# Kernel tuning notes

Hardware: AMD Instinct MI355X
Metric: run time of the kernel (lower is better)

## Reference

```python
import jax, jax.numpy as jnp
import numpy as np

BATCH, SEQ, VOCAB, EMB, UNITS = 128, 80, 10000, 100, 2048

def setup_inputs() -> dict:
    key = jax.random.key(0)
    ks = jax.random.split(key, 12)
    s = 0.02
    return {
        "tokens": jax.random.randint(ks[0], (BATCH, SEQ), 0, VOCAB, dtype=jnp.int32),
        "emb": jax.random.normal(ks[1], (VOCAB, EMB), jnp.float32) * s,
        "W0": jax.random.normal(ks[2], (EMB, 4 * UNITS), jnp.float32) * s,
        "U0": jax.random.normal(ks[3], (UNITS, 4 * UNITS), jnp.float32) * s,
        "b0": jnp.zeros((4 * UNITS,), jnp.float32),
        "W1": jax.random.normal(ks[4], (UNITS, 4 * UNITS), jnp.float32) * s,
        "U1": jax.random.normal(ks[5], (UNITS, 4 * UNITS), jnp.float32) * s,
        "b1": jnp.zeros((4 * UNITS,), jnp.float32),
        "Wd": jax.random.normal(ks[6], (UNITS, UNITS), jnp.float32) * s,
        "bd": jnp.zeros((UNITS,), jnp.float32),
        "Wo": jax.random.normal(ks[7], (UNITS, 1), jnp.float32) * s,
        "bo": jnp.zeros((1,), jnp.float32),
    }

def _lstm_step(x, h, c, W, U, b):
    # Keras LSTMCell gate order: i, f, g(candidate), o
    z = x @ W + h @ U + b  # [B, 4U]
    i, f, g, o = jnp.split(z, 4, axis=-1)
    c_new = jax.nn.sigmoid(f) * c + jax.nn.sigmoid(i) * jnp.tanh(g)
    h_new = jax.nn.sigmoid(o) * jnp.tanh(c_new)
    return h_new, c_new

def reference(tokens, emb, W0, U0, b0, W1, U1, b1, Wd, bd, Wo, bo):
    x = emb[tokens]                      # [B, T, E]
    xs = jnp.swapaxes(x, 0, 1)           # [T, B, E] for scan over time
    B = tokens.shape[0]
    U = U0.shape[0]
    init = (jnp.zeros((B, U), x.dtype), jnp.zeros((B, U), x.dtype),
            jnp.zeros((B, U), x.dtype), jnp.zeros((B, U), x.dtype))

    def step(carry, xt):
        h0, c0, h1, c1 = carry
        h0, c0 = _lstm_step(xt, h0, c0, W0, U0, b0)
        h1, c1 = _lstm_step(h0, h1, c1, W1, U1, b1)
        return (h0, c0, h1, c1), None

    (h0, c0, h1, c1), _ = jax.lax.scan(step, init, xs)
    # out layer: Dense(units) -> Dropout(inference: identity) -> ReLU -> Dense(1)
    y = jax.nn.relu(h1 @ Wd + bd)
    logit = y @ Wo + bo                  # [B, 1]
    return jax.nn.sigmoid(logit)
```

## Files before the change

### kernel.cpp

```cpp
#include <hip/hip_runtime.h>
#include <hip/hip_bf16.h>
#include <hip/hip_fp8.h>
#include <cstdint>

#define B_   128
#define T_   80
#define E_   100
#define U_   2048
#define G4_  8192

#define SA_    16.0f
#define SB4_   64.0f
#define INV_S_ (1.0f / 1024.0f)
#define SCL1_  0x7F7F7F7F

typedef __attribute__((ext_vector_type(4))) float f32x4;
typedef __attribute__((ext_vector_type(8))) int   i32x8;
typedef __attribute__((ext_vector_type(4))) int   i32x4;

__device__ __forceinline__ unsigned char f2fp8(float x) {
    __hip_fp8_e4m3 q(x);
    return q.__x;
}

__device__ __forceinline__ unsigned int q4(float x) {
    float a = fabsf(x);
    unsigned int s = (x < 0.f) ? 8u : 0u;
    unsigned int c = a < 0.25f ? 0u : a < 0.75f ? 1u : a < 1.25f ? 2u :
                     a < 1.75f ? 3u : a < 2.5f  ? 4u : a < 3.5f  ? 5u :
                     a < 5.0f  ? 6u : 7u;
    return s | c;
}

__device__ __forceinline__ unsigned char pk4(float v0, float v1) {
#if __has_builtin(__builtin_amdgcn_cvt_scalef32_pk_fp4_f32)
    unsigned int w = __builtin_amdgcn_cvt_scalef32_pk_fp4_f32(0u, v0, v1, 1.0f, 0);
    return (unsigned char)(w & 0xFF);
#else
    return (unsigned char)(q4(v0) | (q4(v1) << 4));
#endif
}

__global__ __launch_bounds__(256)
void embed_pack(const int* __restrict__ tokens, const float* __restrict__ emb,
                unsigned char* __restrict__ Xp) {
    int gtid = blockIdx.x * 256 + threadIdx.x;
    if (gtid >= T_ * 8 * 64 * 4) return;
    int eb   = gtid & 3;
    int lane = (gtid >> 2) & 63;
    int mtg  = (gtid >> 8) & 7;
    int t    = gtid >> 11;
    int row  = (mtg >> 2) * 64 + (mtg & 3) * 16 + (lane & 15);
    const float* erow = emb + (size_t)tokens[row * T_ + t] * E_;
    unsigned char v[8];
#pragma unroll
    for (int j = 0; j < 8; ++j) {
        int k = (lane >> 4) * 32 + eb * 8 + j;
        v[j] = (k < E_) ? f2fp8(SA_ * erow[k]) : 0;
    }
    unsigned char* dst = Xp + ((size_t)(t * 8 + mtg)) * 2048 + lane * 32 + eb * 8;
    *reinterpret_cast<uint2*>(dst) = *reinterpret_cast<const uint2*>(v);
}

__global__ __launch_bounds__(256)
void pack_all(const float* __restrict__ W0, const float* __restrict__ U0,
              const float* __restrict__ W1, const float* __restrict__ U1,
              const float* __restrict__ Wd,
              unsigned char* __restrict__ W0p, unsigned char* __restrict__ U0p,
              unsigned char* __restrict__ W1p, unsigned char* __restrict__ U1p,
              unsigned char* __restrict__ Wdp) {
    __shared__ float4 st4[32][65];
    const float* stf = reinterpret_cast<const float*>(&st4[0][0]);
    const int tid = threadIdx.x;
    int blk = blockIdx.x;
    const float* W; int K, Ncols, NG, NW; unsigned char* out; int lb;
    if (blk < 2048)      { W = U0; K = U_; Ncols = G4_; NG = 4; NW = 16; out = U0p; lb = blk; }
    else if (blk < 4096) { W = W1; K = U_; Ncols = G4_; NG = 4; NW = 16; out = W1p; lb = blk - 2048; }
    else if (blk < 6144) { W = U1; K = U_; Ncols = G4_; NG = 4; NW = 16; out = U1p; lb = blk - 4096; }
    else if (blk < 6272) { W = W0; K = E_; Ncols = G4_; NG = 4; NW = 1;  out = W0p; lb = blk - 6144; }
    else                 { W = Wd; K = U_; Ncols = U_;  NG = 1; NW = 16; out = Wdp; lb = blk - 6272; }

    int Wm, kg, cg;
    if (NW == 1) { Wm = 0;        kg = lb & 3;         cg = lb >> 2; }
    else         { Wm = lb & 15;  kg = (lb >> 4) & 3;  cg = lb >> 6; }
    int g, utb;
    if (NG == 4) { g = cg >> 3; utb = (cg & 7) * 16; }
    else         { g = 0;       utb = cg * 16; }
    const int cb = cg * 256;

    {
        const int c4 = tid & 63;
        const int r0 = tid >> 6;
        float4 v[8];
#pragma unroll
        for (int p = 0; p < 8; ++p) {
            const int r = p * 4 + r0;
            const int k = Wm * 128 + kg * 32 + r;
            v[p] = make_float4(0.f, 0.f, 0.f, 0.f);
            if (k < K)
                v[p] = *reinterpret_cast<const float4*>(W + (size_t)k * Ncols + cb + c4 * 4);
        }
#pragma unroll
        for (int p = 0; p < 8; ++p) st4[p * 4 + r0][c4] = v[p];
    }
    __syncthreads();

    const int ut_l = tid >> 4;
    const int cl   = tid & 15;
    unsigned char v[16];
#pragma unroll
    for (int b = 0; b < 16; ++b) {
        float v0 = stf[((2 * b)     * 65 + (tid >> 2)) * 4 + (tid & 3)];
        float v1 = stf[((2 * b + 1) * 65 + (tid >> 2)) * 4 + (tid & 3)];
        v[b] = pk4(SB4_ * v0, SB4_ * v1);
    }
    const int ut = utb + ut_l;
    unsigned char* dst = out + (((size_t)(ut * NW + Wm)) * NG + g) * 1024 + (kg * 16 + cl) * 16;
    *reinterpret_cast<uint4*>(dst) = *reinterpret_cast<const uint4*>(v);
}

template<int NW0, int NW1>
__device__ __forceinline__ void ld_set(
    const unsigned char* __restrict__ a0, const unsigned char* __restrict__ a1,
    const unsigned char* __restrict__ b0, const unsigned char* __restrict__ b1,
    int w, i32x8 (&A)[4], i32x4 (&Bv)[4])
{
    if (w < NW0) {
#pragma unroll
        for (int mt = 0; mt < 4; ++mt)
            A[mt] = *reinterpret_cast<const i32x8*>(a0 + (size_t)(mt * NW0 + w) * 2048);
#pragma unroll
        for (int g = 0; g < 4; ++g)
            Bv[g] = *reinterpret_cast<const i32x4*>(b0 + (size_t)(w * 4 + g) * 1024);
    } else {
        int ww = w - NW0;
#pragma unroll
        for (int mt = 0; mt < 4; ++mt)
            A[mt] = *reinterpret_cast<const i32x8*>(a1 + (size_t)(mt * NW1 + ww) * 2048);
#pragma unroll
        for (int g = 0; g < 4; ++g)
            Bv[g] = *reinterpret_cast<const i32x4*>(b1 + (size_t)(ww * 4 + g) * 1024);
    }
}

__device__ __forceinline__ void ld_A(const unsigned char* __restrict__ a,
                                     int stride_nw, int w, i32x8 (&A)[4]) {
#pragma unroll
    for (int mt = 0; mt < 4; ++mt)
        A[mt] = *reinterpret_cast<const i32x8*>(a + (size_t)(mt * stride_nw + w) * 2048);
}

__device__ __forceinline__ void ld_B(const unsigned char* __restrict__ b,
                                     int w, i32x4 (&Bv)[4]) {
#pragma unroll
    for (int g = 0; g < 4; ++g)
        Bv[g] = *reinterpret_cast<const i32x4*>(b + (size_t)(w * 4 + g) * 1024);
}

__device__ __forceinline__ void mfma_set(f32x4 (&acc)[4][4], i32x8 (&A)[4], i32x4 (&Bv)[4]) {
    __builtin_amdgcn_s_setprio(1);
#pragma unroll
    for (int g = 0; g < 4; ++g) {
        i32x8 bf = {Bv[g][0], Bv[g][1], Bv[g][2], Bv[g][3], 0, 0, 0, 0};
#pragma unroll
        for (int mt = 0; mt < 4; ++mt)
            acc[g][mt] = __builtin_amdgcn_mfma_scale_f32_16x16x128_f8f6f4(
                A[mt], bf, acc[g][mt], 0, 4, 0, SCL1_, 0, SCL1_);
    }
    __builtin_amdgcn_s_setprio(0);
}

__device__ __forceinline__ void epilogue(
    f32x4 (&acc)[4][4], const float* __restrict__ bias,
    float* __restrict__ c, unsigned char* __restrict__ h_out,
    float (*zs)[4][64][17], int ut, int mh, int tid, int lane, int kq)
{
    const int lr = tid >> 3;
    const int u0 = (tid & 7) * 2;

    __syncthreads();
#pragma unroll
    for (int g = 0; g < 4; ++g)
#pragma unroll
        for (int mt = 0; mt < 4; ++mt)
#pragma unroll
            for (int r = 0; r < 4; ++r)
                zs[kq][g][mt * 16 + (lane >> 4) * 4 + r][lane & 15] = acc[g][mt][r];
    __syncthreads();

    float zg2[4][2];
#pragma unroll
    for (int g = 0; g < 4; ++g) {
        float s0 = 0.f, s1 = 0.f;
#pragma unroll
        for (int w8 = 0; w8 < 8; ++w8) {
            s0 += zs[w8][g][lr][u0];
            s1 += zs[w8][g][lr][u0 + 1];
        }
        zg2[g][0] = s0;
        zg2[g][1] = s1;
    }

    const int grow = mh * 64 + lr;
    const int unit = ut * 16 + u0;
    const float2 bi  = *reinterpret_cast<const float2*>(&bias[unit]);
    const float2 bfv = *reinterpret_cast<const float2*>(&bias[U_ + unit]);
    const float2 bgv = *reinterpret_cast<const float2*>(&bias[2 * U_ + unit]);
    const float2 bov = *reinterpret_cast<const float2*>(&bias[3 * U_ + unit]);
    float2 cv = *reinterpret_cast<float2*>(&c[(size_t)grow * U_ + unit]);

    float cn[2];
    unsigned char hv[2];
#pragma unroll
    for (int e = 0; e < 2; ++e) {
        float zi = zg2[0][e] * INV_S_ + (e ? bi.y : bi.x);
        float zf = zg2[1][e] * INV_S_ + (e ? bfv.y : bfv.x);
        float zg = zg2[2][e] * INV_S_ + (e ? bgv.y : bgv.x);
        float zo = zg2[3][e] * INV_S_ + (e ? bov.y : bov.x);
        float si = 1.f / (1.f + __expf(-zi));
        float sf = 1.f / (1.f + __expf(-zf));
        float so = 1.f / (1.f + __expf(-zo));
        float tg = tanhf(zg);
        float cc = sf * (e ? cv.y : cv.x) + si * tg;
        cn[e] = cc;
        hv[e] = f2fp8(SA_ * so * tanhf(cc));
    }
    *reinterpret_cast<float2*>(&c[(size_t)grow * U_ + unit]) = make_float2(cn[0], cn[1]);

    const int mt = lr >> 4;
    const int cl = lr & 15;
    const int Wh = unit >> 7;
    const int lg = (unit >> 5) & 3;
    const int e0 = unit & 31;
    size_t fr = (size_t)(mh * 4 + mt) * 16 + Wh;
    uchar2 hv2; hv2.x = hv[0]; hv2.y = hv[1];
    *reinterpret_cast<uchar2*>(&h_out[fr * 2048 + (lg * 16 + cl) * 32 + e0]) = hv2;
}

__global__ __launch_bounds__(512)
void lstm_l0_first(const unsigned char* __restrict__ Xp,
                   const unsigned char* __restrict__ W0p,
                   const unsigned char* __restrict__ U0p,
                   const float* __restrict__ b0,
                   float* __restrict__ c0,
                   const unsigned char* __restrict__ h0zero,
                   unsigned char* __restrict__ h0out) {
    __shared__ float zs[8][4][64][17];
    const int tid  = threadIdx.x;
    const int lane = tid & 63;
    const int kq   = tid >> 6;
    const int b    = blockIdx.x;
    const int s    = b >> 3;
    const int ut   = (b & 7) * 16 + (s >> 1);
    const int mh   = s & 1;

    const unsigned char* a0 = Xp     + ((size_t)(mh * 4) * 1)  * 2048 + lane * 32;
    const unsigned char* a1 = h0zero + ((size_t)(mh * 4) * 16) * 2048 + lane * 32;
    const unsigned char* p0 = W0p + ((size_t)(ut * 1)  * 4) * 1024 + lane * 16;
    const unsigned char* p1 = U0p + ((size_t)(ut * 16) * 4) * 1024 + lane * 16;

    f32x4 acc[4][4];
#pragma unroll
    for (int g = 0; g < 4; ++g)
#pragma unroll
        for (int mt = 0; mt < 4; ++mt) acc[g][mt] = f32x4{0.f, 0.f, 0.f, 0.f};

    i32x8 A0s[4], A1s[4], A2s[4];
    i32x4 B0s[4], B1s[4], B2s[4];
    ld_set<1, 16>(a0, a1, p0, p1, kq, A0s, B0s);
    ld_set<1, 16>(a0, a1, p0, p1, kq + 8, A1s, B1s);
    const bool tail = (kq + 16 < 17);
    if (tail) ld_set<1, 16>(a0, a1, p0, p1, kq + 16, A2s, B2s);
    mfma_set(acc, A0s, B0s);
    mfma_set(acc, A1s, B1s);
    if (tail) mfma_set(acc, A2s, B2s);

    epilogue(acc, b0, c0, h0out, zs, ut, mh, tid, lane, kq);
}

__global__ __launch_bounds__(512)
void lstm_phase(const unsigned char* __restrict__ Xp,
                const unsigned char* __restrict__ W0p,
                const unsigned char* __restrict__ U0p,
                const unsigned char* __restrict__ W1p,
                const unsigned char* __restrict__ U1p,
                const float* __restrict__ b0,
                const float* __restrict__ b1,
                float* __restrict__ c0, float* __restrict__ c1,
                const unsigned char* __restrict__ h0cur,
                unsigned char* __restrict__ h0next,
                const unsigned char* __restrict__ h1in,
                unsigned char* __restrict__ h1out,
                int k) {
    __shared__ float zs[8][4][64][17];
    const int tid  = threadIdx.x;
    const int lane = tid & 63;
    const int kq   = tid >> 6;
    const int b    = blockIdx.x;
    const int s    = b >> 3;
    const int ut   = (b & 7) * 16 + (s >> 1);
    const int mh   = s & 1;
    const bool hasL0 = (k + 1 < T_);

    const unsigned char* a0 = h0cur + ((size_t)(mh * 4) * 16) * 2048 + lane * 32;
    const unsigned char* a1 = h1in  + ((size_t)(mh * 4) * 16) * 2048 + lane * 32;
    const unsigned char* p0 = W1p + ((size_t)(ut * 16) * 4) * 1024 + lane * 16;
    const unsigned char* p1 = U1p + ((size_t)(ut * 16) * 4) * 1024 + lane * 16;
    const unsigned char* l0x  = Xp + (size_t)(k + 1) * 8 * 2048
                                   + ((size_t)(mh * 4) * 1) * 2048 + lane * 32;
    const unsigned char* l0b0 = W0p + ((size_t)(ut * 1)  * 4) * 1024 + lane * 16;
    const unsigned char* l0b1 = U0p + ((size_t)(ut * 16) * 4) * 1024 + lane * 16;

    f32x4 acc[4][4];
#pragma unroll
    for (int g = 0; g < 4; ++g)
#pragma unroll
        for (int mt = 0; mt < 4; ++mt) acc[g][mt] = f32x4{0.f, 0.f, 0.f, 0.f};

    i32x8 A0s[4], A1s[4], A2s[4], A3s[4];
    i32x4 B0s[4], B1s[4];
    ld_A(a0, 16, kq, A0s);       ld_B(p0, kq, B0s);
    ld_A(a0, 16, kq + 8, A1s);   ld_B(p0, kq + 8, B1s);
    ld_A(a1, 16, kq, A2s);
    mfma_set(acc, A0s, B0s);
    ld_B(p1, kq, B0s);
    ld_A(a1, 16, kq + 8, A3s);
    mfma_set(acc, A1s, B1s);
    ld_B(p1, kq + 8, B1s);
    mfma_set(acc, A2s, B0s);
    mfma_set(acc, A3s, B1s);

    i32x4 PB0[4], PB1[4], PBX[4];
    i32x8 PAX[4];
    if (hasL0) {
        ld_B(l0b1, kq, PB0);
        ld_B(l0b1, kq + 8, PB1);
        if (kq == 0) {
            ld_A(l0x, 1, 0, PAX);
            ld_B(l0b0, 0, PBX);
        }
    }

    epilogue(acc, b1, c1, h1out, zs, ut, mh, tid, lane, kq);

    if (hasL0) {
#pragma unroll
        for (int g = 0; g < 4; ++g)
#pragma unroll
            for (int mt = 0; mt < 4; ++mt) acc[g][mt] = f32x4{0.f, 0.f, 0.f, 0.f};

        mfma_set(acc, A0s, PB0);
        mfma_set(acc, A1s, PB1);
        if (kq == 0) mfma_set(acc, PAX, PBX);

        epilogue(acc, b0, c0, h0next, zs, ut, mh, tid, lane, kq);
    }
}

__global__ __launch_bounds__(256)
void head_mfma(const unsigned char* __restrict__ h1p,
               const unsigned char* __restrict__ Wdp,
               const float* __restrict__ bd, float* __restrict__ y) {
    const int lane = threadIdx.x & 63;
    const int w    = threadIdx.x >> 6;
    const int ut   = blockIdx.x & 127;
    const int mh   = blockIdx.x >> 7;

    const unsigned char* ap = h1p + ((size_t)(mh * 4) * 16) * 2048 + lane * 32;
    const unsigned char* wp = Wdp + ((size_t)(ut * 16)) * 1024 + lane * 16;

    f32x4 acc[4];
#pragma unroll
    for (int mt = 0; mt < 4; ++mt) acc[mt] = f32x4{0.f, 0.f, 0.f, 0.f};

#pragma unroll
    for (int wi = 0; wi < 4; ++wi) {
        const int W = w + wi * 4;
        i32x4 bq = *reinterpret_cast<const i32x4*>(wp + (size_t)W * 1024);
        i32x8 bf = {bq[0], bq[1], bq[2], bq[3], 0, 0, 0, 0};
#pragma unroll
        for (int mt = 0; mt < 4; ++mt) {
            i32x8 a = *reinterpret_cast<const i32x8*>(ap + (size_t)(mt * 16 + W) * 2048);
            acc[mt] = __builtin_amdgcn_mfma_scale_f32_16x16x128_f8f6f4(
                a, bf, acc[mt], 0, 4, 0, SCL1_, 0, SCL1_);
        }
    }

    __shared__ float zs[4][64][17];
#pragma unroll
    for (int mt = 0; mt < 4; ++mt)
#pragma unroll
        for (int r = 0; r < 4; ++r)
            zs[w][mt * 16 + (lane >> 4) * 4 + r][lane & 15] = acc[mt][r];
    __syncthreads();

    const int tid = threadIdx.x;
    const int lr  = tid >> 2;
    const int u4  = (tid & 3) * 4;
    const int grow = mh * 64 + lr;
    const int gu   = ut * 16 + u4;

    float4 r;
    float* rr = &r.x;
#pragma unroll
    for (int e = 0; e < 4; ++e) {
        float v = (zs[0][lr][u4 + e] + zs[1][lr][u4 + e] +
                   zs[2][lr][u4 + e] + zs[3][lr][u4 + e]) * INV_S_ + bd[gu + e];
        rr[e] = v > 0.f ? v : 0.f;
    }
    *reinterpret_cast<float4*>(&y[(size_t)grow * U_ + gu]) = r;
}

__global__ __launch_bounds__(256)
void head2(const float* __restrict__ y, const float* __restrict__ Wo,
           const float* __restrict__ bo, float* __restrict__ out) {
    __shared__ float red[256];
    const int b = blockIdx.x;
    const int tid = threadIdx.x;
    float s = 0.f;
    for (int u = tid; u < U_; u += 256) s += y[(size_t)b * U_ + u] * Wo[u];
    red[tid] = s;
    __syncthreads();
    for (int off = 128; off > 0; off >>= 1) {
        if (tid < off) red[tid] += red[tid + off];
        __syncthreads();
    }
    if (tid == 0) out[b] = 1.f / (1.f + __expf(-(red[0] + bo[0])));
}

extern "C" void kernel_launch(void* const* d_in, const int* in_sizes, int n_in,
                              void* d_out, int out_size, void* d_ws, size_t ws_size,
                              hipStream_t stream) {
    const int*   tokens = (const int*)  d_in[0];
    const float* emb    = (const float*)d_in[1];
    const float* W0     = (const float*)d_in[2];
    const float* U0     = (const float*)d_in[3];
    const float* b0     = (const float*)d_in[4];
    const float* W1     = (const float*)d_in[5];
    const float* U1     = (const float*)d_in[6];
    const float* b1     = (const float*)d_in[7];
    const float* Wd     = (const float*)d_in[8];
    const float* bd     = (const float*)d_in[9];
    const float* Wo     = (const float*)d_in[10];
    const float* bo     = (const float*)d_in[11];

    char* base = (char*)d_ws;
    unsigned char* h0a = (unsigned char*)(base + 0);
    unsigned char* h1a = (unsigned char*)(base + 262144);
    float*         c0  = (float*)        (base + 524288);
    float*         c1  = (float*)        (base + 1572864);
    unsigned char* h0b = (unsigned char*)(base + 2621440);
    unsigned char* h1b = (unsigned char*)(base + 2883584);
    unsigned char* Xp  = (unsigned char*)(base + 3145728);
    float*         yb  = (float*)        (base + 3145728);
    unsigned char* W0p = (unsigned char*)(base + 4456448);
    unsigned char* U0p = (unsigned char*)(base + 4980736);
    unsigned char* W1p = (unsigned char*)(base + 13369344);
    unsigned char* U1p = (unsigned char*)(base + 21757952);
    unsigned char* Wdp = (unsigned char*)(base + 30146560);

    hipMemsetAsync(d_ws, 0, 2621440, stream);

    embed_pack<<<(T_ * 8 * 64 * 4 + 255) / 256, 256, 0, stream>>>(tokens, emb, Xp);
    pack_all<<<6784, 256, 0, stream>>>(W0, U0, W1, U1, Wd,
                                       W0p, U0p, W1p, U1p, Wdp);

    lstm_l0_first<<<256, 512, 0, stream>>>(Xp, W0p, U0p, b0, c0, h0a, h0b);

    for (int k = 0; k < T_; ++k) {
        const unsigned char* h0cur  = (k & 1) ? h0a : h0b;
        unsigned char*       h0next = (k & 1) ? h0b : h0a;
        const unsigned char* h1in   = (k & 1) ? h1b : h1a;
        unsigned char*       h1out  = (k & 1) ? h1a : h1b;
        lstm_phase<<<256, 512, 0, stream>>>(Xp, W0p, U0p, W1p, U1p,
                                            b0, b1, c0, c1,
                                            h0cur, h0next, h1in, h1out, k);
    }
    head_mfma<<<256, 256, 0, stream>>>(h1a, Wdp, bd, yb);
    head2<<<B_, 256, 0, stream>>>(yb, Wo, bo, (float*)d_out);
}
```

Measured before the change: 1.044 ms.

## Quantize hidden states to FP4 and skip zero-state matmul in first step

Hidden states h0/h1 are now stored as packed FP4 (e2m1) with a larger scale instead of FP8, halving their bytes, and all recurrent and head MFMAs use the fp4×fp4 mode. The x-projection path stays FP8 and is rescaled by a constant to match the new accumulator scale. The first layer-0 step drops the U0·h multiply against the all-zero initial state. This cuts per-step load traffic and register footprint for A operands but coarsens hidden-state precision, which may hurt accuracy.

```diff
diff --git a/kernel.cpp b/kernel.cpp
--- a/kernel.cpp
+++ b/kernel.cpp
@@ -10,8 +10,10 @@
 #define G4_  8192
 
 #define SA_    16.0f
+#define SA4_   128.0f
 #define SB4_   64.0f
-#define INV_S_ (1.0f / 1024.0f)
+#define INV_S_ (1.0f / 8192.0f)
+#define RXUP_  8.0f
 #define SCL1_  0x7F7F7F7F
 
 typedef __attribute__((ext_vector_type(4))) float f32x4;
@@ -119,35 +121,18 @@
     *reinterpret_cast<uint4*>(dst) = *reinterpret_cast<const uint4*>(v);
 }
 
-template<int NW0, int NW1>
-__device__ __forceinline__ void ld_set(
-    const unsigned char* __restrict__ a0, const unsigned char* __restrict__ a1,
-    const unsigned char* __restrict__ b0, const unsigned char* __restrict__ b1,
-    int w, i32x8 (&A)[4], i32x4 (&Bv)[4])
-{
-    if (w < NW0) {
-#pragma unroll
-        for (int mt = 0; mt < 4; ++mt)
-            A[mt] = *reinterpret_cast<const i32x8*>(a0 + (size_t)(mt * NW0 + w) * 2048);
-#pragma unroll
-        for (int g = 0; g < 4; ++g)
-            Bv[g] = *reinterpret_cast<const i32x4*>(b0 + (size_t)(w * 4 + g) * 1024);
-    } else {
-        int ww = w - NW0;
-#pragma unroll
-        for (int mt = 0; mt < 4; ++mt)
-            A[mt] = *reinterpret_cast<const i32x8*>(a1 + (size_t)(mt * NW1 + ww) * 2048);
-#pragma unroll
-        for (int g = 0; g < 4; ++g)
-            Bv[g] = *reinterpret_cast<const i32x4*>(b1 + (size_t)(ww * 4 + g) * 1024);
-    }
-}
-
 __device__ __forceinline__ void ld_A(const unsigned char* __restrict__ a,
                                      int stride_nw, int w, i32x8 (&A)[4]) {
 #pragma unroll
     for (int mt = 0; mt < 4; ++mt)
         A[mt] = *reinterpret_cast<const i32x8*>(a + (size_t)(mt * stride_nw + w) * 2048);
+}
+
+__device__ __forceinline__ void ld_A4(const unsigned char* __restrict__ a,
+                                      int stride_nw, int w, i32x4 (&A)[4]) {
+#pragma unroll
+    for (int mt = 0; mt < 4; ++mt)
+        A[mt] = *reinterpret_cast<const i32x4*>(a + (size_t)(mt * stride_nw + w) * 1024);
 }
 
 __device__ __forceinline__ void ld_B(const unsigned char* __restrict__ b,
@@ -166,6 +151,21 @@
         for (int mt = 0; mt < 4; ++mt)
             acc[g][mt] = __builtin_amdgcn_mfma_scale_f32_16x16x128_f8f6f4(
                 A[mt], bf, acc[g][mt], 0, 4, 0, SCL1_, 0, SCL1_);
+    }
+    __builtin_amdgcn_s_setprio(0);
+}
+
+__device__ __forceinline__ void mfma_set44(f32x4 (&acc)[4][4], i32x4 (&A)[4], i32x4 (&Bv)[4]) {
+    __builtin_amdgcn_s_setprio(1);
+#pragma unroll
+    for (int g = 0; g < 4; ++g) {
+        i32x8 bf = {Bv[g][0], Bv[g][1], Bv[g][2], Bv[g][3], 0, 0, 0, 0};
+#pragma unroll
+        for (int mt = 0; mt < 4; ++mt) {
+            i32x8 af = {A[mt][0], A[mt][1], A[mt][2], A[mt][3], 0, 0, 0, 0};
+            acc[g][mt] = __builtin_amdgcn_mfma_scale_f32_16x16x128_f8f6f4(
+                af, bf, acc[g][mt], 4, 4, 0, SCL1_, 0, SCL1_);
+        }
     }
     __builtin_amdgcn_s_setprio(0);
 }
@@ -209,8 +209,7 @@
     const float2 bov = *reinterpret_cast<const float2*>(&bias[3 * U_ + unit]);
     float2 cv = *reinterpret_cast<float2*>(&c[(size_t)grow * U_ + unit]);
 
-    float cn[2];
-    unsigned char hv[2];
+    float cn[2], hf[2];
 #pragma unroll
     for (int e = 0; e < 2; ++e) {
         float zi = zg2[0][e] * INV_S_ + (e ? bi.y : bi.x);
@@ -223,27 +222,24 @@
         float tg = tanhf(zg);
         float cc = sf * (e ? cv.y : cv.x) + si * tg;
         cn[e] = cc;
-        hv[e] = f2fp8(SA_ * so * tanhf(cc));
+        hf[e] = so * tanhf(cc);
     }
     *reinterpret_cast<float2*>(&c[(size_t)grow * U_ + unit]) = make_float2(cn[0], cn[1]);
 
-    const int mt = lr >> 4;
-    const int cl = lr & 15;
-    const int Wh = unit >> 7;
-    const int lg = (unit >> 5) & 3;
-    const int e0 = unit & 31;
+    const int mt  = lr >> 4;
+    const int cl  = lr & 15;
+    const int Wh  = unit >> 7;
+    const int lgg = (unit >> 5) & 3;
     size_t fr = (size_t)(mh * 4 + mt) * 16 + Wh;
-    uchar2 hv2; hv2.x = hv[0]; hv2.y = hv[1];
-    *reinterpret_cast<uchar2*>(&h_out[fr * 2048 + (lg * 16 + cl) * 32 + e0]) = hv2;
+    h_out[fr * 1024 + (lgg * 16 + cl) * 16 + ((unit & 31) >> 1)] =
+        pk4(SA4_ * hf[0], SA4_ * hf[1]);
 }
 
 __global__ __launch_bounds__(512)
 void lstm_l0_first(const unsigned char* __restrict__ Xp,
                    const unsigned char* __restrict__ W0p,
-                   const unsigned char* __restrict__ U0p,
                    const float* __restrict__ b0,
                    float* __restrict__ c0,
-                   const unsigned char* __restrict__ h0zero,
                    unsigned char* __restrict__ h0out) {
     __shared__ float zs[8][4][64][17];
     const int tid  = threadIdx.x;
@@ -254,26 +250,27 @@
     const int ut   = (b & 7) * 16 + (s >> 1);
     const int mh   = s & 1;
 
-    const unsigned char* a0 = Xp     + ((size_t)(mh * 4) * 1)  * 2048 + lane * 32;
-    const unsigned char* a1 = h0zero + ((size_t)(mh * 4) * 16) * 2048 + lane * 32;
-    const unsigned char* p0 = W0p + ((size_t)(ut * 1)  * 4) * 1024 + lane * 16;
-    const unsigned char* p1 = U0p + ((size_t)(ut * 16) * 4) * 1024 + lane * 16;
-
     f32x4 acc[4][4];
 #pragma unroll
     for (int g = 0; g < 4; ++g)
 #pragma unroll
         for (int mt = 0; mt < 4; ++mt) acc[g][mt] = f32x4{0.f, 0.f, 0.f, 0.f};
 
-    i32x8 A0s[4], A1s[4], A2s[4];
-    i32x4 B0s[4], B1s[4], B2s[4];
-    ld_set<1, 16>(a0, a1, p0, p1, kq, A0s, B0s);
-    ld_set<1, 16>(a0, a1, p0, p1, kq + 8, A1s, B1s);
-    const bool tail = (kq + 16 < 17);
-    if (tail) ld_set<1, 16>(a0, a1, p0, p1, kq + 16, A2s, B2s);
-    mfma_set(acc, A0s, B0s);
-    mfma_set(acc, A1s, B1s);
-    if (tail) mfma_set(acc, A2s, B2s);
+    if (kq == 0) {
+        const unsigned char* l0x  = Xp + ((size_t)(mh * 4) * 1) * 2048 + lane * 32;
+        const unsigned char* l0b0 = W0p + ((size_t)(ut * 1) * 4) * 1024 + lane * 16;
+        i32x8 PAX[4];
+        i32x4 PBX[4];
+        ld_A(l0x, 1, 0, PAX);
+        ld_B(l0b0, 0, PBX);
+        mfma_set(acc, PAX, PBX);
+#pragma unroll
+        for (int g = 0; g < 4; ++g)
+#pragma unroll
+            for (int mt = 0; mt < 4; ++mt)
+#pragma unroll
+                for (int r = 0; r < 4; ++r) acc[g][mt][r] *= RXUP_;
+    }
 
     epilogue(acc, b0, c0, h0out, zs, ut, mh, tid, lane, kq);
 }
@@ -302,8 +299,8 @@
     const int mh   = s & 1;
     const bool hasL0 = (k + 1 < T_);
 
-    const unsigned char* a0 = h0cur + ((size_t)(mh * 4) * 16) * 2048 + lane * 32;
-    const unsigned char* a1 = h1in  + ((size_t)(mh * 4) * 16) * 2048 + lane * 32;
+    const unsigned char* a0 = h0cur + ((size_t)(mh * 4) * 16) * 1024 + lane * 16;
+    const unsigned char* a1 = h1in  + ((size_t)(mh * 4) * 16) * 1024 + lane * 16;
     const unsigned char* p0 = W1p + ((size_t)(ut * 16) * 4) * 1024 + lane * 16;
     const unsigned char* p1 = U1p + ((size_t)(ut * 16) * 4) * 1024 + lane * 16;
     const unsigned char* l0x  = Xp + (size_t)(k + 1) * 8 * 2048
@@ -317,18 +314,18 @@
 #pragma unroll
         for (int mt = 0; mt < 4; ++mt) acc[g][mt] = f32x4{0.f, 0.f, 0.f, 0.f};
 
-    i32x8 A0s[4], A1s[4], A2s[4], A3s[4];
+    i32x4 A0s[4], A1s[4], A2s[4], A3s[4];
     i32x4 B0s[4], B1s[4];
-    ld_A(a0, 16, kq, A0s);       ld_B(p0, kq, B0s);
-    ld_A(a0, 16, kq + 8, A1s);   ld_B(p0, kq + 8, B1s);
-    ld_A(a1, 16, kq, A2s);
-    mfma_set(acc, A0s, B0s);
+    ld_A4(a0, 16, kq, A0s);       ld_B(p0, kq, B0s);
+    ld_A4(a0, 16, kq + 8, A1s);   ld_B(p0, kq + 8, B1s);
+    ld_A4(a1, 16, kq, A2s);
+    mfma_set44(acc, A0s, B0s);
     ld_B(p1, kq, B0s);
-    ld_A(a1, 16, kq + 8, A3s);
-    mfma_set(acc, A1s, B1s);
+    ld_A4(a1, 16, kq + 8, A3s);
+    mfma_set44(acc, A1s, B1s);
     ld_B(p1, kq + 8, B1s);
-    mfma_set(acc, A2s, B0s);
-    mfma_set(acc, A3s, B1s);
+    mfma_set44(acc, A2s, B0s);
+    mfma_set44(acc, A3s, B1s);
 
     i32x4 PB0[4], PB1[4], PBX[4];
     i32x8 PAX[4];
@@ -349,9 +346,17 @@
 #pragma unroll
             for (int mt = 0; mt < 4; ++mt) acc[g][mt] = f32x4{0.f, 0.f, 0.f, 0.f};
 
-        mfma_set(acc, A0s, PB0);
-        mfma_set(acc, A1s, PB1);
-        if (kq == 0) mfma_set(acc, PAX, PBX);
+        if (kq == 0) {
+            mfma_set(acc, PAX, PBX);
+#pragma unroll
+            for (int g = 0; g < 4; ++g)
+#pragma unroll
+                for (int mt = 0; mt < 4; ++mt)
+#pragma unroll
+                    for (int r = 0; r < 4; ++r) acc[g][mt][r] *= RXUP_;
+        }
+        mfma_set44(acc, A0s, PB0);
+        mfma_set44(acc, A1s, PB1);
 
         epilogue(acc, b0, c0, h0next, zs, ut, mh, tid, lane, kq);
     }
@@ -366,7 +371,7 @@
     const int ut   = blockIdx.x & 127;
     const int mh   = blockIdx.x >> 7;
 
-    const unsigned char* ap = h1p + ((size_t)(mh * 4) * 16) * 2048 + lane * 32;
+    const unsigned char* ap = h1p + ((size_t)(mh * 4) * 16) * 1024 + lane * 16;
     const unsigned char* wp = Wdp + ((size_t)(ut * 16)) * 1024 + lane * 16;
 
     f32x4 acc[4];
@@ -380,9 +385,10 @@
         i32x8 bf = {bq[0], bq[1], bq[2], bq[3], 0, 0, 0, 0};
 #pragma unroll
         for (int mt = 0; mt < 4; ++mt) {
-            i32x8 a = *reinterpret_cast<const i32x8*>(ap + (size_t)(mt * 16 + W) * 2048);
+            i32x4 aq = *reinterpret_cast<const i32x4*>(ap + (size_t)(mt * 16 + W) * 1024);
+            i32x8 af = {aq[0], aq[1], aq[2], aq[3], 0, 0, 0, 0};
             acc[mt] = __builtin_amdgcn_mfma_scale_f32_16x16x128_f8f6f4(
-                a, bf, acc[mt], 0, 4, 0, SCL1_, 0, SCL1_);
+                af, bf, acc[mt], 4, 4, 0, SCL1_, 0, SCL1_);
         }
     }
 
@@ -465,7 +471,7 @@
     pack_all<<<6784, 256, 0, stream>>>(W0, U0, W1, U1, Wd,
                                        W0p, U0p, W1p, U1p, Wdp);
 
-    lstm_l0_first<<<256, 512, 0, stream>>>(Xp, W0p, U0p, b0, c0, h0a, h0b);
+    lstm_l0_first<<<256, 512, 0, stream>>>(Xp, W0p, b0, c0, h0b);
 
     for (int k = 0; k < T_; ++k) {
         const unsigned char* h0cur  = (k & 1) ? h0a : h0b;
```

Result: faster. 904.9 us (-13.4%).
